# Kernel optimization log

Hardware: AMD Instinct MI355X
Metric: run time of the kernel (lower is better)

## Reference

```python
import jax, jax.numpy as jnp
import numpy as np

P = 32    # num_particles
B = 64    # batch_size
T = 100   # seq_len
W = 50    # window_length
E = 64    # act embedding dim (emb_obs=0)
H = 256   # hidden_dim
ALPHA = 0.5  # resamp_alpha


def setup_inputs() -> dict:
    key = jax.random.key(0)
    ks = jax.random.split(key, 12)
    def lin(k, fan_in, shape):
        return jax.random.normal(k, shape, jnp.float32) / np.sqrt(fan_in).astype(np.float32)
    u = jax.random.uniform(ks[4], (T, B, P, P), jnp.float32, 1e-6, 1.0 - 1e-6)
    return {
        "prev_window": jax.random.normal(ks[0], (B, T, W), jnp.float32),
        "h0": jax.random.uniform(ks[1], (P * B, H), jnp.float32),
        "c0": jax.random.uniform(ks[2], (P * B, H), jnp.float32),
        "eps": jax.random.normal(ks[3], (T, P * B, H), jnp.float32),
        "gumbel": -jnp.log(-jnp.log(u)),  # Gumbel noise for multinomial resampling
        "W_act": lin(ks[5], W, (W, E)), "b_act": jnp.zeros((E,), jnp.float32),
        "W_ih": lin(ks[6], E, (E, 5 * H)), "b_ih": jnp.zeros((5 * H,), jnp.float32),
        "W_hh": lin(ks[7], H, (H, 5 * H)), "b_hh": jnp.zeros((5 * H,), jnp.float32),
        "W_obs": lin(ks[8], H + E, (H + E, 1)), "b_obs": jnp.zeros((1,), jnp.float32),
        "W_lab": lin(ks[9], H, (H, 1)), "b_lab": jnp.zeros((1,), jnp.float32),
    }


def reference(prev_window, h0, c0, eps, gumbel, W_act, b_act, W_ih, b_ih,
              W_hh, b_hh, W_obs, b_obs, W_lab, b_lab):
    # act embedding, tiled over particles (particle-major, matching torch repeat)
    emb = jax.nn.relu(prev_window @ W_act + b_act)          # [B,T,E]
    xs = jnp.swapaxes(jnp.tile(emb, (P, 1, 1)), 0, 1)       # [T,P*B,E]
    p0 = jnp.full((P * B, 1), np.log(1.0 / P), jnp.float32)

    barange = jnp.arange(B)

    def step(carry, inputs):
        h, c, p = carry                                      # [PB,H],[PB,H],[PB,1]
        x, eps_t, g_t = inputs                               # [PB,E],[PB,H],[B,P,P]
        gates = x @ W_ih + b_ih + h @ W_hh + b_hh            # [PB,5H]
        i, f, g, o, var = jnp.split(gates, 5, axis=1)
        mu = jax.nn.sigmoid(f) * c + jax.nn.sigmoid(i) * jnp.tanh(g)
        c1 = mu + jax.nn.softplus(var) * eps_t               # stochastic cell (reparameterize)
        h1 = jax.nn.sigmoid(o) * jnp.tanh(c1)
        # observation log-likelihood per particle
        logpdf = jnp.concatenate([h1, x], axis=1) @ W_obs + b_obs  # [PB,1]
        p1 = jax.nn.log_softmax((p + logpdf).reshape(P, B), axis=0)  # [P,B]
        # soft resampling: q = alpha*w + (1-alpha)/P, sample via Gumbel-argmax
        w1 = jnp.exp(p1)
        logits = jnp.log(ALPHA * w1 + (1.0 - ALPHA) / P)     # [P_src,B]
        idx = jnp.argmax(logits.T[:, None, :] + g_t, axis=-1).T  # [P_new,B]
        h_new = h1.reshape(P, B, H)[idx, barange[None, :]]   # [P,B,H]
        c_new = c1.reshape(P, B, H)[idx, barange[None, :]]
        w = w1[idx, barange[None, :]]                        # [P,B]
        w = w / (ALPHA * w + (1.0 - ALPHA) / P)              # importance correction
        p_new = jax.nn.log_softmax(jnp.log(w), axis=0)
        h_new = h_new.reshape(P * B, H)
        c_new = c_new.reshape(P * B, H)
        p_new = p_new.reshape(P * B, 1)
        return (h_new, c_new, p_new), (h_new, p_new)

    _, (hs, ps) = jax.lax.scan(step, (h0, c0, p0), (xs, eps, gumbel))
    # hs: [T,PB,H], ps: [T,PB,1]; dropout rate 0 -> identity
    prob = ps.reshape(T, P, B, 1)
    out = hs.reshape(T, P, B, H)
    y = jnp.sum(out * jnp.exp(prob), axis=1)                 # weighted particle mean [T,B,H]
    y_out = jax.nn.sigmoid(y @ W_lab + b_lab)                # [T,B,1]
    pf_out = jax.nn.sigmoid(hs @ W_lab + b_lab)              # [T,PB,1]
    return y_out, pf_out
```

## Files before the change

### kernel.cpp

```cpp
#include <hip/hip_runtime.h>
#include <hip/hip_bf16.h>
#include <cstddef>
#include <cstdint>

#define PP 32
#define BB 64
#define TT 100
#define WW 50
#define EE 64
#define HH 256

typedef float f4 __attribute__((ext_vector_type(4)));
typedef __attribute__((ext_vector_type(8))) short short8;
typedef __attribute__((ext_vector_type(4))) float f32x4;

__device__ __forceinline__ float sigm(float x) { return 1.0f / (1.0f + expf(-x)); }
__device__ __forceinline__ float splus(float x) {
    return fmaxf(x, 0.0f) + log1pf(expf(-fabsf(x)));
}
__device__ __forceinline__ unsigned short bfh(float x) {
    __hip_bfloat16 h = __float2bfloat16(x);
    return *reinterpret_cast<unsigned short*>(&h);
}
__device__ __forceinline__ float bff(unsigned short u) {
    __hip_bfloat16 h; *reinterpret_cast<unsigned short*>(&h) = u;
    return __bfloat162float(h);
}

__global__ __launch_bounds__(256) void k_emb(
    const float* __restrict__ pw, const float* __restrict__ w_act,
    const float* __restrict__ b_act, const float* __restrict__ w_obs,
    const float* __restrict__ b_obs,
    unsigned short* __restrict__ embh, unsigned short* __restrict__ embl,
    float* __restrict__ xobs)
{
    int tid = threadIdx.x;
    int sub = tid >> 6;
    int e   = tid & 63;
    int bt  = blockIdx.x * 4 + sub;
    int b = bt / TT, t = bt % TT;

    __shared__ float pws[4][WW + 2];
    if (e < WW) pws[sub][e] = pw[(size_t)bt * WW + e];
    __syncthreads();

    float acc = b_act[e];
    #pragma unroll 5
    for (int w = 0; w < WW; ++w) acc += pws[sub][w] * w_act[w * EE + e];
    float r = fmaxf(acc, 0.0f);

    unsigned short uh = bfh(r);
    embh[((size_t)t * BB + b) * EE + e] = uh;
    embl[((size_t)t * BB + b) * EE + e] = bfh(r - bff(uh));

    float xv = r * w_obs[HH + e];
    #pragma unroll
    for (int d = 1; d < 64; d <<= 1) xv += __shfl_xor(xv, d);
    if (e == 0) xobs[t * BB + b] = xv + b_obs[0];
}

__global__ __launch_bounds__(256) void k_packB(
    const float* __restrict__ W_ih, const float* __restrict__ W_hh,
    unsigned short* __restrict__ Bp)
{
    int i = blockIdx.x * 256 + threadIdx.x;
    int colp = i / 51200;  int r = i - colp * 51200;
    int bidx = r / 2560;   r -= bidx * 2560;
    int g    = r / 512;    r -= g * 512;
    int lane = r >> 3;     int e = r & 7;

    int c = (bidx < 10) ? bidx : (bidx - 10);
    int k = c * 32 + (lane >> 4) * 8 + e;
    int col = g * HH + colp * 16 + (lane & 15);
    float w = (k < HH) ? W_hh[(size_t)k * 1280 + col]
                       : W_ih[(size_t)(k - HH) * 1280 + col];
    unsigned short uh = bfh(w);
    Bp[i] = (bidx < 10) ? uh : bfh(w - bff(uh));
}

__global__ __launch_bounds__(256) void k_split0(
    const float* __restrict__ h0, const float* __restrict__ c0,
    unsigned short* __restrict__ hh, unsigned short* __restrict__ hl,
    float* __restrict__ cc)
{
    int i = blockIdx.x * 256 + threadIdx.x;
    float v = h0[i];
    unsigned short uh = bfh(v);
    hh[i] = uh;
    hl[i] = bfh(v - bff(uh));
    cc[i] = c0[i];
}

__global__ __launch_bounds__(256, 2) void s1_mfma(
    const unsigned short* __restrict__ Bp,
    const unsigned short* __restrict__ embh_t, const unsigned short* __restrict__ embl_t,
    const unsigned short* __restrict__ hh_in, const unsigned short* __restrict__ hl_in,
    const float* __restrict__ c_in,
    unsigned short* __restrict__ hh_out, unsigned short* __restrict__ hl_out,
    float* __restrict__ c_out,
    const int* __restrict__ gidx,
    const float* __restrict__ b_ih, const float* __restrict__ b_hh,
    const float* __restrict__ w_obs, const float* __restrict__ w_lab,
    const float* __restrict__ eps_t,
    float* __restrict__ dpo, float* __restrict__ dpl)
{
    __shared__ short8 BhL[3200];

    const int tid  = threadIdx.x;
    const int rp   = blockIdx.x & 31;
    const int cp   = blockIdx.x >> 5;
    const int lane = tid & 63;
    const int w    = tid >> 6;
    const int lh   = lane & 15;
    const int kq   = lane >> 4;
    const int R0   = rp * 64 + w * 16;

    {
        const short8* src = (const short8*)Bp + (size_t)cp * 6400;
        for (int s = tid; s < 3200; s += 256) BhL[s] = src[s];
    }

    const int myrow = R0 + lh;
    const int sr    = gidx ? gidx[myrow] : myrow;
    const size_t hoff = (size_t)sr * 512 + (size_t)kq * 16;
    const size_t eoff = (size_t)(myrow & 63) * 128 + (size_t)kq * 16;

    f32x4 acc[5];
    #pragma unroll
    for (int g = 0; g < 5; ++g) acc[g] = (f32x4)(0.0f);

    const char* hhp = (const char*)hh_in  + hoff;
    const char* hlp = (const char*)hl_in  + hoff;
    const char* ehp = (const char*)embh_t + eoff;
    const char* elp = (const char*)embl_t + eoff;
    const short8* bslab = (const short8*)Bp + (size_t)cp * 6400 + lane;

    __syncthreads();

    #pragma unroll
    for (int cs = 0; cs < 10; ++cs) {
        short8 Ah, Al;
        if (cs < 8) {
            Ah = *(const short8*)(hhp + cs * 64);
            Al = *(const short8*)(hlp + cs * 64);
        } else {
            Ah = *(const short8*)(ehp + (cs - 8) * 64);
            Al = *(const short8*)(elp + (cs - 8) * 64);
        }
        short8 Bh[5], Bl[5];
        #pragma unroll
        for (int g = 0; g < 5; ++g) {
            Bh[g] = BhL[(cs * 5 + g) * 64 + lane];
            Bl[g] = bslab[((cs + 10) * 5 + g) * 64];
        }
        #pragma unroll
        for (int g = 0; g < 5; ++g)
            acc[g] = __builtin_amdgcn_mfma_f32_16x16x32_bf16(Ah, Bh[g], acc[g], 0, 0, 0);
        #pragma unroll
        for (int g = 0; g < 5; ++g)
            acc[g] = __builtin_amdgcn_mfma_f32_16x16x32_bf16(Ah, Bl[g], acc[g], 0, 0, 0);
        #pragma unroll
        for (int g = 0; g < 5; ++g)
            acc[g] = __builtin_amdgcn_mfma_f32_16x16x32_bf16(Al, Bh[g], acc[g], 0, 0, 0);
    }

    const int hcol = cp * 16 + lh;
    float bsum[5];
    #pragma unroll
    for (int g = 0; g < 5; ++g) bsum[g] = b_ih[g * HH + hcol] + b_hh[g * HH + hcol];
    const float wobs_l = w_obs[hcol];
    const float wlab_l = w_lab[hcol];

    #pragma unroll
    for (int reg = 0; reg < 4; ++reg) {
        int row = R0 + kq * 4 + reg;
        int sr2 = gidx ? gidx[row] : row;
        float cpv = c_in[(size_t)sr2 * HH + hcol];
        float ep  = eps_t[(size_t)row * HH + hcol];

        float gi = acc[0][reg] + bsum[0];
        float gf = acc[1][reg] + bsum[1];
        float gg = acc[2][reg] + bsum[2];
        float go = acc[3][reg] + bsum[3];
        float gv = acc[4][reg] + bsum[4];

        float mu  = sigm(gf) * cpv + sigm(gi) * tanhf(gg);
        float c1v = mu + splus(gv) * ep;
        float h1v = sigm(go) * tanhf(c1v);

        c_out[(size_t)row * HH + hcol] = c1v;
        unsigned short uh = bfh(h1v);
        hh_out[(size_t)row * HH + hcol] = uh;
        hl_out[(size_t)row * HH + hcol] = bfh(h1v - bff(uh));

        float po = h1v * wobs_l, pl = h1v * wlab_l;
        po += __shfl_xor(po, 1); po += __shfl_xor(po, 2);
        po += __shfl_xor(po, 4); po += __shfl_xor(po, 8);
        pl += __shfl_xor(pl, 1); pl += __shfl_xor(pl, 2);
        pl += __shfl_xor(pl, 4); pl += __shfl_xor(pl, 8);
        if (lh == 0) {
            dpo[cp * 2048 + row] = po;
            dpl[cp * 2048 + row] = pl;
        }
    }
}

__global__ __launch_bounds__(256) void s2_kernel(
    const float* __restrict__ dpo, const float* __restrict__ dpl,
    const float* __restrict__ xobs_t, const float* __restrict__ g_t,
    const float* __restrict__ b_lab,
    float* __restrict__ p_buf, int first,
    int* __restrict__ gidx_next,
    float* __restrict__ y_out_t, float* __restrict__ pf_out_t)
{
    int b   = blockIdx.x;
    int tid = threadIdx.x;

    __shared__ float gt[PP][PP + 1];
    __shared__ float lg[PP];
    __shared__ float w1s[PP];
    __shared__ float lgt[PP];
    __shared__ float pnew[PP];
    __shared__ float dpart[PP];
    __shared__ int   idxs[PP];

    {
        f4 v = ((const f4*)(g_t + (size_t)b * 1024))[tid];
        int p = tid >> 3, j0 = (tid & 7) * 4;
        gt[p][j0 + 0] = v.x; gt[p][j0 + 1] = v.y;
        gt[p][j0 + 2] = v.z; gt[p][j0 + 3] = v.w;
    }

    int p = tid >> 3, j = tid & 7;
    {
        int o = p * BB + b;
        float s = dpo[j * 2048 + o] + dpo[(j + 8) * 2048 + o];
        s += __shfl_xor(s, 1); s += __shfl_xor(s, 2); s += __shfl_xor(s, 4);
        if (j == 0) {
            float pprev = first ? -3.4657359027997265f : p_buf[o];
            lg[p] = pprev + s + xobs_t[b];
        }
    }
    __syncthreads();

    if (tid < 32) {
        float v = lg[tid];
        float m = v;
        #pragma unroll
        for (int d = 1; d < 32; d <<= 1) m = fmaxf(m, __shfl_xor(m, d));
        float e = expf(v - m), se = e;
        #pragma unroll
        for (int d = 1; d < 32; d <<= 1) se += __shfl_xor(se, d);
        float l1 = v - m - logf(se);
        float w1 = expf(l1);
        w1s[tid] = w1;
        lgt[tid] = logf(0.5f * w1 + 0.015625f);
    }
    __syncthreads();

    if (tid < 32) {
        int p2 = tid;
        float best = -INFINITY; int bi = 0;
        #pragma unroll 8
        for (int jj = 0; jj < 32; ++jj) {
            float val = lgt[jj] + gt[p2][jj];
            if (val > best) { best = val; bi = jj; }
        }
        idxs[p2] = bi;
        gidx_next[p2 * BB + b] = bi * BB + b;

        float wv = w1s[bi];
        wv = wv / (0.5f * wv + 0.015625f);
        float lw = logf(wv);
        float m2 = lw;
        #pragma unroll
        for (int d = 1; d < 32; d <<= 1) m2 = fmaxf(m2, __shfl_xor(m2, d));
        float e2 = expf(lw - m2), s2 = e2;
        #pragma unroll
        for (int d = 1; d < 32; d <<= 1) s2 += __shfl_xor(s2, d);
        float pn = lw - m2 - logf(s2);
        pnew[p2] = pn;
        p_buf[p2 * BB + b] = pn;
    }
    __syncthreads();

    {
        int src = idxs[p] * BB + b;
        float d = dpl[j * 2048 + src] + dpl[(j + 8) * 2048 + src];
        d += __shfl_xor(d, 1); d += __shfl_xor(d, 2); d += __shfl_xor(d, 4);
        if (j == 0) dpart[p] = d;
    }
    __syncthreads();

    if (tid < 32) {
        float dd = dpart[tid];
        float bl = b_lab[0];
        pf_out_t[tid * BB + b] = 1.0f / (1.0f + expf(-(dd + bl)));
        float contrib = expf(pnew[tid]) * dd;
        #pragma unroll
        for (int d = 1; d < 32; d <<= 1) contrib += __shfl_xor(contrib, d);
        if (tid == 0) y_out_t[b] = 1.0f / (1.0f + expf(-(contrib + bl)));
    }
}

extern "C" void kernel_launch(void* const* d_in, const int* in_sizes, int n_in,
                              void* d_out, int out_size, void* d_ws, size_t ws_size,
                              hipStream_t stream)
{
    const float* prev_window = (const float*)d_in[0];
    const float* h0    = (const float*)d_in[1];
    const float* c0    = (const float*)d_in[2];
    const float* eps   = (const float*)d_in[3];
    const float* gum   = (const float*)d_in[4];
    const float* W_act = (const float*)d_in[5];
    const float* b_act = (const float*)d_in[6];
    const float* W_ih  = (const float*)d_in[7];
    const float* b_ih  = (const float*)d_in[8];
    const float* W_hh  = (const float*)d_in[9];
    const float* b_hh  = (const float*)d_in[10];
    const float* W_obs = (const float*)d_in[11];
    const float* b_obs = (const float*)d_in[12];
    const float* W_lab = (const float*)d_in[13];
    const float* b_lab = (const float*)d_in[14];

    float* out = (float*)d_out;
    char* w = (char*)d_ws;

    unsigned short* Bp   = (unsigned short*)(w);
    unsigned short* embh = (unsigned short*)(w + 1638400);
    unsigned short* embl = (unsigned short*)(w + 2457600);
    unsigned short* hhA  = (unsigned short*)(w + 3276800);
    unsigned short* hlA  = (unsigned short*)(w + 4325376);
    unsigned short* hhB  = (unsigned short*)(w + 5373952);
    unsigned short* hlB  = (unsigned short*)(w + 6422528);
    float*  cA   = (float*)(w + 7471104);
    float*  cB   = (float*)(w + 9568256);
    float*  xobs = (float*)(w + 11665408);
    float*  pbuf = (float*)(w + 11691008);
    int*    gidx = (int*)(w + 11699200);
    float*  dpo  = (float*)(w + 11707392);
    float*  dpl  = (float*)(w + 11838464);

    k_emb<<<1600, 256, 0, stream>>>(prev_window, W_act, b_act, W_obs, b_obs,
                                    embh, embl, xobs);
    k_packB<<<3200, 256, 0, stream>>>(W_ih, W_hh, Bp);
    k_split0<<<2048, 256, 0, stream>>>(h0, c0, hhA, hlA, cA);

    for (int t = 0; t < TT; ++t) {
        const unsigned short* hh_in = (t & 1) ? hhB : hhA;
        const unsigned short* hl_in = (t & 1) ? hlB : hlA;
        const float*          c_in  = (t & 1) ? cB  : cA;
        unsigned short* hh_out = (t & 1) ? hhA : hhB;
        unsigned short* hl_out = (t & 1) ? hlA : hlB;
        float*          c_out  = (t & 1) ? cA  : cB;

        s1_mfma<<<512, 256, 0, stream>>>(
            Bp, embh + (size_t)t * 4096, embl + (size_t)t * 4096,
            hh_in, hl_in, c_in, hh_out, hl_out, c_out,
            (t == 0) ? nullptr : gidx,
            b_ih, b_hh, W_obs, W_lab,
            eps + (size_t)t * 524288,
            dpo, dpl);

        s2_kernel<<<64, 256, 0, stream>>>(
            dpo, dpl, xobs + t * BB, gum + (size_t)t * 65536,
            b_lab, pbuf, (t == 0) ? 1 : 0, gidx,
            out + (size_t)t * BB,
            out + (size_t)TT * BB + (size_t)t * PP * BB);
    }
}
```

Before: 2.405 ms.

## Precompute input-gate projection x@W_ih for all timesteps outside the recurrence

The embedding contribution to the gates does not depend on the recurrent state and is identical across particles, so it is now computed once per timestep and batch in fp32 by a new pre-pass kernel. The per-step MFMA kernel then runs 8 K-chunks instead of 10 and adds the precomputed term in its epilogue. This cuts the per-step matrix work and the shared-memory B slab, and the input term is now exact fp32 rather than split-bf16. The trade-offs are an extra kernel launch up front, a larger workspace (about 33 MB), and an extra global read of the precomputed values per step.

```diff
diff --git a/kernel.cpp b/kernel.cpp
--- a/kernel.cpp
+++ b/kernel.cpp
@@ -31,8 +31,7 @@
     const float* __restrict__ pw, const float* __restrict__ w_act,
     const float* __restrict__ b_act, const float* __restrict__ w_obs,
     const float* __restrict__ b_obs,
-    unsigned short* __restrict__ embh, unsigned short* __restrict__ embl,
-    float* __restrict__ xobs)
+    float* __restrict__ emb, float* __restrict__ xobs)
 {
     int tid = threadIdx.x;
     int sub = tid >> 6;
@@ -48,15 +47,58 @@
     #pragma unroll 5
     for (int w = 0; w < WW; ++w) acc += pws[sub][w] * w_act[w * EE + e];
     float r = fmaxf(acc, 0.0f);
-
-    unsigned short uh = bfh(r);
-    embh[((size_t)t * BB + b) * EE + e] = uh;
-    embl[((size_t)t * BB + b) * EE + e] = bfh(r - bff(uh));
+    emb[((size_t)t * BB + b) * EE + e] = r;
 
     float xv = r * w_obs[HH + e];
     #pragma unroll
     for (int d = 1; d < 64; d <<= 1) xv += __shfl_xor(xv, d);
     if (e == 0) xobs[t * BB + b] = xv + b_obs[0];
+}
+
+__global__ __launch_bounds__(256) void k_embW(
+    const float* __restrict__ emb, const float* __restrict__ W_ih,
+    float* __restrict__ embW)
+{
+    int t  = blockIdx.x / 16;
+    int cp = blockIdx.x - (blockIdx.x / 16) * 16;
+    int tid = threadIdx.x;
+
+    __shared__ float le[64][65];
+    __shared__ float lw[64][80];
+
+    {
+        const f4* src = (const f4*)(emb + (size_t)t * 4096);
+        for (int i = tid; i < 1024; i += 256) {
+            f4 v = src[i];
+            int b = i >> 4, e0 = (i & 15) * 4;
+            le[b][e0 + 0] = v.x; le[b][e0 + 1] = v.y;
+            le[b][e0 + 2] = v.z; le[b][e0 + 3] = v.w;
+        }
+    }
+    {
+        for (int i = tid; i < 5120; i += 256) {
+            int e = i / 80, c = i - e * 80;
+            int g = c >> 4, lh = c & 15;
+            lw[e][c] = W_ih[(size_t)e * 1280 + g * 256 + cp * 16 + lh];
+        }
+    }
+    __syncthreads();
+
+    int lh = tid & 15, bq = tid >> 4;
+    #pragma unroll
+    for (int g = 0; g < 5; ++g) {
+        float a0 = 0, a1 = 0, a2 = 0, a3 = 0;
+        #pragma unroll
+        for (int e = 0; e < 64; ++e) {
+            float wv = lw[e][g * 16 + lh];
+            a0 += le[bq * 4 + 0][e] * wv;
+            a1 += le[bq * 4 + 1][e] * wv;
+            a2 += le[bq * 4 + 2][e] * wv;
+            a3 += le[bq * 4 + 3][e] * wv;
+        }
+        f4 o = {a0, a1, a2, a3};
+        *(f4*)&embW[(((size_t)t * 16 + cp) * 5 + g) * 1024 + lh * 64 + bq * 4] = o;
+    }
 }
 
 __global__ __launch_bounds__(256) void k_packB(
@@ -93,7 +135,7 @@
 
 __global__ __launch_bounds__(256, 2) void s1_mfma(
     const unsigned short* __restrict__ Bp,
-    const unsigned short* __restrict__ embh_t, const unsigned short* __restrict__ embl_t,
+    const float* __restrict__ embW_t,
     const unsigned short* __restrict__ hh_in, const unsigned short* __restrict__ hl_in,
     const float* __restrict__ c_in,
     unsigned short* __restrict__ hh_out, unsigned short* __restrict__ hl_out,
@@ -104,7 +146,7 @@
     const float* __restrict__ eps_t,
     float* __restrict__ dpo, float* __restrict__ dpl)
 {
-    __shared__ short8 BhL[3200];
+    __shared__ short8 BhL[2560];
 
     const int tid  = threadIdx.x;
     const int rp   = blockIdx.x & 31;
@@ -117,36 +159,27 @@
 
     {
         const short8* src = (const short8*)Bp + (size_t)cp * 6400;
-        for (int s = tid; s < 3200; s += 256) BhL[s] = src[s];
+        for (int s = tid; s < 2560; s += 256) BhL[s] = src[s];
     }
 
     const int myrow = R0 + lh;
     const int sr    = gidx ? gidx[myrow] : myrow;
     const size_t hoff = (size_t)sr * 512 + (size_t)kq * 16;
-    const size_t eoff = (size_t)(myrow & 63) * 128 + (size_t)kq * 16;
 
     f32x4 acc[5];
     #pragma unroll
     for (int g = 0; g < 5; ++g) acc[g] = (f32x4)(0.0f);
 
-    const char* hhp = (const char*)hh_in  + hoff;
-    const char* hlp = (const char*)hl_in  + hoff;
-    const char* ehp = (const char*)embh_t + eoff;
-    const char* elp = (const char*)embl_t + eoff;
+    const char* hhp = (const char*)hh_in + hoff;
+    const char* hlp = (const char*)hl_in + hoff;
     const short8* bslab = (const short8*)Bp + (size_t)cp * 6400 + lane;
 
     __syncthreads();
 
     #pragma unroll
-    for (int cs = 0; cs < 10; ++cs) {
-        short8 Ah, Al;
-        if (cs < 8) {
-            Ah = *(const short8*)(hhp + cs * 64);
-            Al = *(const short8*)(hlp + cs * 64);
-        } else {
-            Ah = *(const short8*)(ehp + (cs - 8) * 64);
-            Al = *(const short8*)(elp + (cs - 8) * 64);
-        }
+    for (int cs = 0; cs < 8; ++cs) {
+        short8 Ah = *(const short8*)(hhp + cs * 64);
+        short8 Al = *(const short8*)(hlp + cs * 64);
         short8 Bh[5], Bl[5];
         #pragma unroll
         for (int g = 0; g < 5; ++g) {
@@ -170,6 +203,11 @@
     for (int g = 0; g < 5; ++g) bsum[g] = b_ih[g * HH + hcol] + b_hh[g * HH + hcol];
     const float wobs_l = w_obs[hcol];
     const float wlab_l = w_lab[hcol];
+
+    f4 ew[5];
+    #pragma unroll
+    for (int g = 0; g < 5; ++g)
+        ew[g] = *(const f4*)&embW_t[((size_t)cp * 5 + g) * 1024 + lh * 64 + w * 16 + kq * 4];
 
     #pragma unroll
     for (int reg = 0; reg < 4; ++reg) {
@@ -178,11 +216,11 @@
         float cpv = c_in[(size_t)sr2 * HH + hcol];
         float ep  = eps_t[(size_t)row * HH + hcol];
 
-        float gi = acc[0][reg] + bsum[0];
-        float gf = acc[1][reg] + bsum[1];
-        float gg = acc[2][reg] + bsum[2];
-        float go = acc[3][reg] + bsum[3];
-        float gv = acc[4][reg] + bsum[4];
+        float gi = acc[0][reg] + bsum[0] + ew[0][reg];
+        float gf = acc[1][reg] + bsum[1] + ew[1][reg];
+        float gg = acc[2][reg] + bsum[2] + ew[2][reg];
+        float go = acc[3][reg] + bsum[3] + ew[3][reg];
+        float gv = acc[4][reg] + bsum[4] + ew[4][reg];
 
         float mu  = sigm(gf) * cpv + sigm(gi) * tanhf(gg);
         float c1v = mu + splus(gv) * ep;
@@ -327,22 +365,23 @@
     char* w = (char*)d_ws;
 
     unsigned short* Bp   = (unsigned short*)(w);
-    unsigned short* embh = (unsigned short*)(w + 1638400);
-    unsigned short* embl = (unsigned short*)(w + 2457600);
-    unsigned short* hhA  = (unsigned short*)(w + 3276800);
-    unsigned short* hlA  = (unsigned short*)(w + 4325376);
-    unsigned short* hhB  = (unsigned short*)(w + 5373952);
-    unsigned short* hlB  = (unsigned short*)(w + 6422528);
-    float*  cA   = (float*)(w + 7471104);
-    float*  cB   = (float*)(w + 9568256);
-    float*  xobs = (float*)(w + 11665408);
-    float*  pbuf = (float*)(w + 11691008);
-    int*    gidx = (int*)(w + 11699200);
-    float*  dpo  = (float*)(w + 11707392);
-    float*  dpl  = (float*)(w + 11838464);
+    float*  emb  = (float*)(w + 1638400);
+    float*  embW = (float*)(w + 3276800);
+    unsigned short* hhA  = (unsigned short*)(w + 36044800);
+    unsigned short* hlA  = (unsigned short*)(w + 37093376);
+    unsigned short* hhB  = (unsigned short*)(w + 38141952);
+    unsigned short* hlB  = (unsigned short*)(w + 39190528);
+    float*  cA   = (float*)(w + 40239104);
+    float*  cB   = (float*)(w + 42336256);
+    float*  xobs = (float*)(w + 44433408);
+    float*  pbuf = (float*)(w + 44459008);
+    int*    gidx = (int*)(w + 44467200);
+    float*  dpo  = (float*)(w + 44475392);
+    float*  dpl  = (float*)(w + 44606464);
 
     k_emb<<<1600, 256, 0, stream>>>(prev_window, W_act, b_act, W_obs, b_obs,
-                                    embh, embl, xobs);
+                                    emb, xobs);
+    k_embW<<<1600, 256, 0, stream>>>(emb, W_ih, embW);
     k_packB<<<3200, 256, 0, stream>>>(W_ih, W_hh, Bp);
     k_split0<<<2048, 256, 0, stream>>>(h0, c0, hhA, hlA, cA);
 
@@ -355,7 +394,7 @@
         float*          c_out  = (t & 1) ? cA  : cB;
 
         s1_mfma<<<512, 256, 0, stream>>>(
-            Bp, embh + (size_t)t * 4096, embl + (size_t)t * 4096,
+            Bp, embW + (size_t)t * 81920,
             hh_in, hl_in, c_in, hh_out, hl_out, c_out,
             (t == 0) ? nullptr : gidx,
             b_ih, b_hh, W_obs, W_lab,
```

New measurement: 2.449 ms. Within noise of the previous version (+1.8%).

## Fuse resampling step into next LSTM step kernel, halving per-step launches

Applied to the files above, without the earlier changes.

The separate per-timestep resampling kernel is removed. Each block of the next step's MFMA kernel now redundantly recomputes the log-softmax and Gumbel-argmax for its own particle row, so it can gather h and c directly without a gidx round-trip. Output writes for step t-1 (pf, y) are spread across designated blocks, and a final s2_fin handles the last step. The partial dot products move to a row-major [row][16] layout with double-buffered dpo/dpl/pbuf. This removes about 100 kernel launches and their serialization, at the cost of redundant softmax and argmax work in all 512 blocks. It also makes the y computation in one block serial, which could lengthen the critical path.

```diff
diff --git a/kernel.cpp b/kernel.cpp
--- a/kernel.cpp
+++ b/kernel.cpp
@@ -91,20 +91,28 @@
     cc[i] = c0[i];
 }
 
-__global__ __launch_bounds__(256, 2) void s1_mfma(
+__global__ __launch_bounds__(256, 2) void g_step(
     const unsigned short* __restrict__ Bp,
     const unsigned short* __restrict__ embh_t, const unsigned short* __restrict__ embl_t,
     const unsigned short* __restrict__ hh_in, const unsigned short* __restrict__ hl_in,
     const float* __restrict__ c_in,
     unsigned short* __restrict__ hh_out, unsigned short* __restrict__ hl_out,
     float* __restrict__ c_out,
-    const int* __restrict__ gidx,
+    const float* __restrict__ dpo_prev, const float* __restrict__ dpl_prev,
+    float* __restrict__ dpo_cur, float* __restrict__ dpl_cur,
+    const float* __restrict__ pb_prev, float* __restrict__ pb_cur,
+    const float* __restrict__ xobs_prev, const float* __restrict__ gum_prev,
     const float* __restrict__ b_ih, const float* __restrict__ b_hh,
     const float* __restrict__ w_obs, const float* __restrict__ w_lab,
+    const float* __restrict__ b_lab,
     const float* __restrict__ eps_t,
-    float* __restrict__ dpo, float* __restrict__ dpl)
+    float* __restrict__ y_prev, float* __restrict__ pf_prev,
+    int skip, int rfirst)
 {
     __shared__ short8 BhL[3200];
+    __shared__ float lgS[PP][65];
+    __shared__ float lgtS[PP][65];
+    __shared__ int   idxS[BB];
 
     const int tid  = threadIdx.x;
     const int rp   = blockIdx.x & 31;
@@ -120,10 +128,107 @@
         for (int s = tid; s < 3200; s += 256) BhL[s] = src[s];
     }
 
-    const int myrow = R0 + lh;
-    const int sr    = gidx ? gidx[myrow] : myrow;
-    const size_t hoff = (size_t)sr * 512 + (size_t)kq * 16;
-    const size_t eoff = (size_t)(myrow & 63) * 128 + (size_t)kq * 16;
+    if (!skip) {
+        #pragma unroll
+        for (int k = 0; k < 8; ++k) {
+            int e = tid + k * 256;
+            int p = e >> 6, b = e & 63;
+            const f4* q = (const f4*)(dpo_prev + (size_t)e * 16);
+            f4 q0 = q[0], q1 = q[1], q2 = q[2], q3 = q[3];
+            float s = ((q0.x+q0.y)+(q0.z+q0.w)) + ((q1.x+q1.y)+(q1.z+q1.w))
+                    + ((q2.x+q2.y)+(q2.z+q2.w)) + ((q3.x+q3.y)+(q3.z+q3.w));
+            float pprev = rfirst ? -3.4657359027997265f : pb_prev[e];
+            lgS[p][b] = pprev + s + xobs_prev[b];
+        }
+        __syncthreads();
+
+        {
+            int half = lane >> 5, pl = lane & 31;
+            #pragma unroll
+            for (int it = 0; it < 8; ++it) {
+                int b = w * 16 + it * 2 + half;
+                float v = lgS[pl][b];
+                float m = v;
+                #pragma unroll
+                for (int d = 1; d < 32; d <<= 1) m = fmaxf(m, __shfl_xor(m, d));
+                float e = expf(v - m), se = e;
+                #pragma unroll
+                for (int d = 1; d < 32; d <<= 1) se += __shfl_xor(se, d);
+                float l1 = v - m - logf(se);
+                float w1 = expf(l1);
+                lgS[pl][b]  = w1;
+                lgtS[pl][b] = logf(0.5f * w1 + 0.015625f);
+            }
+        }
+        __syncthreads();
+
+        {
+            int b = tid >> 2, jq = tid & 3;
+            const float* gb = gum_prev + (size_t)b * 1024 + rp * 32;
+            float best = -INFINITY; int bi = 0;
+            #pragma unroll
+            for (int u = 0; u < 8; ++u) {
+                int jj = jq * 8 + u;
+                float val = lgtS[jj][b] + gb[jj];
+                if (val > best) { best = val; bi = jj; }
+            }
+            #pragma unroll
+            for (int d = 1; d <= 2; d <<= 1) {
+                float ov = __shfl_xor(best, d);
+                int   oj = __shfl_xor(bi, d);
+                if (ov > best || (ov == best && oj < bi)) { best = ov; bi = oj; }
+            }
+            if (jq == 0) idxS[b] = bi;
+        }
+        __syncthreads();
+
+        if (cp == 0 && tid < 64) {
+            int b = tid;
+            float wv = lgS[idxS[b]][b];
+            wv = wv / (0.5f * wv + 0.015625f);
+            pb_cur[rp * 64 + b] = logf(wv);
+        }
+        if (cp == 1) {
+            int b = tid >> 2, cq = tid & 3;
+            int srcrow = idxS[b] * 64 + b;
+            f4 vq = ((const f4*)(dpl_prev + (size_t)srcrow * 16))[cq];
+            float dsum = (vq.x + vq.y) + (vq.z + vq.w);
+            dsum += __shfl_xor(dsum, 1);
+            dsum += __shfl_xor(dsum, 2);
+            if (cq == 0) pf_prev[rp * 64 + b] = 1.0f / (1.0f + expf(-(dsum + b_lab[0])));
+        }
+        if (cp == 2 && rp == 0) {
+            int b = tid >> 2, pq = tid & 3;
+            float aw = 0.0f, ww = 0.0f;
+            for (int u = 0; u < 8; ++u) {
+                int p = pq * 8 + u;
+                const float* gb2 = gum_prev + (size_t)b * 1024 + p * 32;
+                float best = -INFINITY; int bi = 0;
+                for (int jj = 0; jj < 32; ++jj) {
+                    float val = lgtS[jj][b] + gb2[jj];
+                    if (val > best) { best = val; bi = jj; }
+                }
+                float wv = lgS[bi][b];
+                wv = wv / (0.5f * wv + 0.015625f);
+                const f4* q = (const f4*)(dpl_prev + (size_t)(bi * 64 + b) * 16);
+                f4 q0 = q[0], q1 = q[1], q2 = q[2], q3 = q[3];
+                float dsum = ((q0.x+q0.y)+(q0.z+q0.w)) + ((q1.x+q1.y)+(q1.z+q1.w))
+                           + ((q2.x+q2.y)+(q2.z+q2.w)) + ((q3.x+q3.y)+(q3.z+q3.w));
+                aw += wv * dsum; ww += wv;
+            }
+            aw += __shfl_xor(aw, 1); aw += __shfl_xor(aw, 2);
+            ww += __shfl_xor(ww, 1); ww += __shfl_xor(ww, 2);
+            if (pq == 0) y_prev[b] = 1.0f / (1.0f + expf(-(aw / ww + b_lab[0])));
+        }
+    } else {
+        if (tid < 64) idxS[tid] = rp;
+        __syncthreads();
+    }
+
+    const int b_a = w * 16 + lh;
+    const int srr = idxS[b_a] * 64 + b_a;
+    const size_t hoff = (size_t)srr * 512 + (size_t)kq * 16;
+    const size_t eoff = (size_t)b_a * 128 + (size_t)kq * 16;
 
     f32x4 acc[5];
     #pragma unroll
@@ -134,8 +239,6 @@
     const char* ehp = (const char*)embh_t + eoff;
     const char* elp = (const char*)embl_t + eoff;
     const short8* bslab = (const short8*)Bp + (size_t)cp * 6400 + lane;
-
-    __syncthreads();
 
     #pragma unroll
     for (int cs = 0; cs < 10; ++cs) {
@@ -174,7 +277,8 @@
     #pragma unroll
     for (int reg = 0; reg < 4; ++reg) {
         int row = R0 + kq * 4 + reg;
-        int sr2 = gidx ? gidx[row] : row;
+        int b2  = w * 16 + kq * 4 + reg;
+        int sr2 = idxS[b2] * 64 + b2;
         float cpv = c_in[(size_t)sr2 * HH + hcol];
         float ep  = eps_t[(size_t)row * HH + hcol];
 
@@ -199,18 +303,16 @@
         pl += __shfl_xor(pl, 1); pl += __shfl_xor(pl, 2);
         pl += __shfl_xor(pl, 4); pl += __shfl_xor(pl, 8);
         if (lh == 0) {
-            dpo[cp * 2048 + row] = po;
-            dpl[cp * 2048 + row] = pl;
-        }
-    }
-}
-
-__global__ __launch_bounds__(256) void s2_kernel(
+            dpo_cur[row * 16 + cp] = po;
+            dpl_cur[row * 16 + cp] = pl;
+        }
+    }
+}
+
+__global__ __launch_bounds__(256) void s2_fin(
     const float* __restrict__ dpo, const float* __restrict__ dpl,
     const float* __restrict__ xobs_t, const float* __restrict__ g_t,
-    const float* __restrict__ b_lab,
-    float* __restrict__ p_buf, int first,
-    int* __restrict__ gidx_next,
+    const float* __restrict__ b_lab, const float* __restrict__ p_buf,
     float* __restrict__ y_out_t, float* __restrict__ pf_out_t)
 {
     int b   = blockIdx.x;
@@ -234,12 +336,9 @@
     int p = tid >> 3, j = tid & 7;
     {
         int o = p * BB + b;
-        float s = dpo[j * 2048 + o] + dpo[(j + 8) * 2048 + o];
+        float s = dpo[o * 16 + j] + dpo[o * 16 + j + 8];
         s += __shfl_xor(s, 1); s += __shfl_xor(s, 2); s += __shfl_xor(s, 4);
-        if (j == 0) {
-            float pprev = first ? -3.4657359027997265f : p_buf[o];
-            lg[p] = pprev + s + xobs_t[b];
-        }
+        if (j == 0) lg[p] = p_buf[o] + s + xobs_t[b];
     }
     __syncthreads();
 
@@ -267,7 +366,6 @@
             if (val > best) { best = val; bi = jj; }
         }
         idxs[p2] = bi;
-        gidx_next[p2 * BB + b] = bi * BB + b;
 
         float wv = w1s[bi];
         wv = wv / (0.5f * wv + 0.015625f);
@@ -278,15 +376,13 @@
         float e2 = expf(lw - m2), s2 = e2;
         #pragma unroll
         for (int d = 1; d < 32; d <<= 1) s2 += __shfl_xor(s2, d);
-        float pn = lw - m2 - logf(s2);
-        pnew[p2] = pn;
-        p_buf[p2 * BB + b] = pn;
+        pnew[p2] = lw - m2 - logf(s2);
     }
     __syncthreads();
 
     {
         int src = idxs[p] * BB + b;
-        float d = dpl[j * 2048 + src] + dpl[(j + 8) * 2048 + src];
+        float d = dpl[src * 16 + j] + dpl[src * 16 + j + 8];
         d += __shfl_xor(d, 1); d += __shfl_xor(d, 2); d += __shfl_xor(d, 4);
         if (j == 0) dpart[p] = d;
     }
@@ -336,10 +432,12 @@
     float*  cA   = (float*)(w + 7471104);
     float*  cB   = (float*)(w + 9568256);
     float*  xobs = (float*)(w + 11665408);
-    float*  pbuf = (float*)(w + 11691008);
-    int*    gidx = (int*)(w + 11699200);
-    float*  dpo  = (float*)(w + 11707392);
-    float*  dpl  = (float*)(w + 11838464);
+    float*  pbA  = (float*)(w + 11691008);
+    float*  pbB  = (float*)(w + 11699200);
+    float*  dpoA = (float*)(w + 11707392);
+    float*  dpoB = (float*)(w + 11838464);
+    float*  dplA = (float*)(w + 11969536);
+    float*  dplB = (float*)(w + 12100608);
 
     k_emb<<<1600, 256, 0, stream>>>(prev_window, W_act, b_act, W_obs, b_obs,
                                     embh, embl, xobs);
@@ -347,25 +445,37 @@
     k_split0<<<2048, 256, 0, stream>>>(h0, c0, hhA, hlA, cA);
 
     for (int t = 0; t < TT; ++t) {
-        const unsigned short* hh_in = (t & 1) ? hhB : hhA;
-        const unsigned short* hl_in = (t & 1) ? hlB : hlA;
-        const float*          c_in  = (t & 1) ? cB  : cA;
-        unsigned short* hh_out = (t & 1) ? hhA : hhB;
-        unsigned short* hl_out = (t & 1) ? hlA : hlB;
-        float*          c_out  = (t & 1) ? cA  : cB;
-
-        s1_mfma<<<512, 256, 0, stream>>>(
+        int par = t & 1;
+        const unsigned short* hh_in = par ? hhB : hhA;
+        const unsigned short* hl_in = par ? hlB : hlA;
+        const float*          c_in  = par ? cB  : cA;
+        unsigned short* hh_out = par ? hhA : hhB;
+        unsigned short* hl_out = par ? hlA : hlB;
+        float*          c_out  = par ? cA  : cB;
+
+        float* dpoC = par ? dpoB : dpoA;
+        float* dplC = par ? dplB : dplA;
+        const float* dpoP = par ? dpoA : dpoB;
+        const float* dplP = par ? dplA : dplB;
+        float* pbC = par ? pbB : pbA;
+        const float* pbP = par ? pbA : pbB;
+
+        int tp = (t > 0) ? (t - 1) : 0;
+        g_step<<<512, 256, 0, stream>>>(
             Bp, embh + (size_t)t * 4096, embl + (size_t)t * 4096,
             hh_in, hl_in, c_in, hh_out, hl_out, c_out,
-            (t == 0) ? nullptr : gidx,
-            b_ih, b_hh, W_obs, W_lab,
+            dpoP, dplP, dpoC, dplC, pbP, pbC,
+            xobs + tp * BB, gum + (size_t)tp * 65536,
+            b_ih, b_hh, W_obs, W_lab, b_lab,
             eps + (size_t)t * 524288,
-            dpo, dpl);
-
-        s2_kernel<<<64, 256, 0, stream>>>(
-            dpo, dpl, xobs + t * BB, gum + (size_t)t * 65536,
-            b_lab, pbuf, (t == 0) ? 1 : 0, gidx,
-            out + (size_t)t * BB,
-            out + (size_t)TT * BB + (size_t)t * PP * BB);
-    }
-}
+            out + (size_t)tp * BB,
+            out + (size_t)TT * BB + (size_t)tp * PP * BB,
+            (t == 0) ? 1 : 0, (t == 1) ? 1 : 0);
+    }
+
+    s2_fin<<<64, 256, 0, stream>>>(
+        dpoB, dplB, xobs + 99 * BB, gum + (size_t)99 * 65536,
+        b_lab, pbB,
+        out + (size_t)99 * BB,
+        out + (size_t)TT * BB + (size_t)99 * PP * BB);
+}
```

After: 3.269 ms. +35.9%, slower.

## Fuse resampling step into recurrent kernel with atomic-counter grid barrier

Applied to the files above, without the earlier changes.

Merges the per-batch resampling and output kernel into the MFMA LSTM-step kernel. Each block increments a per-timestep atomic counter once its outputs are written. The first 64 blocks spin until all 512 blocks have arrived, then run the resampling logic, which halves the kernel launches per timestep. The loads of the previous cell state and the eps noise are also hoisted ahead of the MFMA loop to hide their latency. The spin-wait relies on all 512 blocks being co-resident; if they are not, the kernel can deadlock.

```diff
diff --git a/kernel.cpp b/kernel.cpp
--- a/kernel.cpp
+++ b/kernel.cpp
@@ -91,20 +91,32 @@
     cc[i] = c0[i];
 }
 
-__global__ __launch_bounds__(256, 2) void s1_mfma(
+__global__ __launch_bounds__(256, 2) void g_step(
     const unsigned short* __restrict__ Bp,
     const unsigned short* __restrict__ embh_t, const unsigned short* __restrict__ embl_t,
     const unsigned short* __restrict__ hh_in, const unsigned short* __restrict__ hl_in,
     const float* __restrict__ c_in,
     unsigned short* __restrict__ hh_out, unsigned short* __restrict__ hl_out,
     float* __restrict__ c_out,
-    const int* __restrict__ gidx,
+    const int* __restrict__ gidx_in,
+    int* __restrict__ gidx_out,
     const float* __restrict__ b_ih, const float* __restrict__ b_hh,
     const float* __restrict__ w_obs, const float* __restrict__ w_lab,
     const float* __restrict__ eps_t,
-    float* __restrict__ dpo, float* __restrict__ dpl)
+    float* __restrict__ dpo, float* __restrict__ dpl,
+    const float* __restrict__ xobs_t, const float* __restrict__ g_t,
+    const float* __restrict__ b_lab, float* __restrict__ p_buf, int first,
+    float* __restrict__ y_out_t, float* __restrict__ pf_out_t,
+    unsigned* __restrict__ cnt)
 {
     __shared__ short8 BhL[3200];
+    __shared__ float s_gt[PP][PP + 1];
+    __shared__ float s_lg[PP];
+    __shared__ float s_w1[PP];
+    __shared__ float s_lgt[PP];
+    __shared__ float s_pn[PP];
+    __shared__ float s_dp[PP];
+    __shared__ int   s_idx[PP];
 
     const int tid  = threadIdx.x;
     const int rp   = blockIdx.x & 31;
@@ -121,9 +133,21 @@
     }
 
     const int myrow = R0 + lh;
-    const int sr    = gidx ? gidx[myrow] : myrow;
+    const int sr    = gidx_in ? gidx_in[myrow] : myrow;
     const size_t hoff = (size_t)sr * 512 + (size_t)kq * 16;
     const size_t eoff = (size_t)(myrow & 63) * 128 + (size_t)kq * 16;
+
+    const int hcol = cp * 16 + lh;
+    int   srow[4];
+    float cpre[4], epre[4];
+    #pragma unroll
+    for (int reg = 0; reg < 4; ++reg) {
+        int row = R0 + kq * 4 + reg;
+        int sr2 = gidx_in ? gidx_in[row] : row;
+        srow[reg] = sr2;
+        cpre[reg] = c_in[(size_t)sr2 * HH + hcol];
+        epre[reg] = eps_t[(size_t)row * HH + hcol];
+    }
 
     f32x4 acc[5];
     #pragma unroll
@@ -164,7 +188,6 @@
             acc[g] = __builtin_amdgcn_mfma_f32_16x16x32_bf16(Al, Bh[g], acc[g], 0, 0, 0);
     }
 
-    const int hcol = cp * 16 + lh;
     float bsum[5];
     #pragma unroll
     for (int g = 0; g < 5; ++g) bsum[g] = b_ih[g * HH + hcol] + b_hh[g * HH + hcol];
@@ -174,9 +197,8 @@
     #pragma unroll
     for (int reg = 0; reg < 4; ++reg) {
         int row = R0 + kq * 4 + reg;
-        int sr2 = gidx ? gidx[row] : row;
-        float cpv = c_in[(size_t)sr2 * HH + hcol];
-        float ep  = eps_t[(size_t)row * HH + hcol];
+        float cpv = cpre[reg];
+        float ep  = epre[reg];
 
         float gi = acc[0][reg] + bsum[0];
         float gf = acc[1][reg] + bsum[1];
@@ -203,103 +225,100 @@
             dpl[cp * 2048 + row] = pl;
         }
     }
-}
-
-__global__ __launch_bounds__(256) void s2_kernel(
-    const float* __restrict__ dpo, const float* __restrict__ dpl,
-    const float* __restrict__ xobs_t, const float* __restrict__ g_t,
-    const float* __restrict__ b_lab,
-    float* __restrict__ p_buf, int first,
-    int* __restrict__ gidx_next,
-    float* __restrict__ y_out_t, float* __restrict__ pf_out_t)
-{
-    int b   = blockIdx.x;
-    int tid = threadIdx.x;
-
-    __shared__ float gt[PP][PP + 1];
-    __shared__ float lg[PP];
-    __shared__ float w1s[PP];
-    __shared__ float lgt[PP];
-    __shared__ float pnew[PP];
-    __shared__ float dpart[PP];
-    __shared__ int   idxs[PP];
-
-    {
-        f4 v = ((const f4*)(g_t + (size_t)b * 1024))[tid];
-        int p = tid >> 3, j0 = (tid & 7) * 4;
-        gt[p][j0 + 0] = v.x; gt[p][j0 + 1] = v.y;
-        gt[p][j0 + 2] = v.z; gt[p][j0 + 3] = v.w;
-    }
-
-    int p = tid >> 3, j = tid & 7;
-    {
-        int o = p * BB + b;
-        float s = dpo[j * 2048 + o] + dpo[(j + 8) * 2048 + o];
-        s += __shfl_xor(s, 1); s += __shfl_xor(s, 2); s += __shfl_xor(s, 4);
-        if (j == 0) {
-            float pprev = first ? -3.4657359027997265f : p_buf[o];
-            lg[p] = pprev + s + xobs_t[b];
-        }
-    }
+
+    __threadfence();
     __syncthreads();
-
-    if (tid < 32) {
-        float v = lg[tid];
-        float m = v;
-        #pragma unroll
-        for (int d = 1; d < 32; d <<= 1) m = fmaxf(m, __shfl_xor(m, d));
-        float e = expf(v - m), se = e;
-        #pragma unroll
-        for (int d = 1; d < 32; d <<= 1) se += __shfl_xor(se, d);
-        float l1 = v - m - logf(se);
-        float w1 = expf(l1);
-        w1s[tid] = w1;
-        lgt[tid] = logf(0.5f * w1 + 0.015625f);
-    }
-    __syncthreads();
-
-    if (tid < 32) {
-        int p2 = tid;
-        float best = -INFINITY; int bi = 0;
-        #pragma unroll 8
-        for (int jj = 0; jj < 32; ++jj) {
-            float val = lgt[jj] + gt[p2][jj];
-            if (val > best) { best = val; bi = jj; }
-        }
-        idxs[p2] = bi;
-        gidx_next[p2 * BB + b] = bi * BB + b;
-
-        float wv = w1s[bi];
-        wv = wv / (0.5f * wv + 0.015625f);
-        float lw = logf(wv);
-        float m2 = lw;
-        #pragma unroll
-        for (int d = 1; d < 32; d <<= 1) m2 = fmaxf(m2, __shfl_xor(m2, d));
-        float e2 = expf(lw - m2), s2 = e2;
-        #pragma unroll
-        for (int d = 1; d < 32; d <<= 1) s2 += __shfl_xor(s2, d);
-        float pn = lw - m2 - logf(s2);
-        pnew[p2] = pn;
-        p_buf[p2 * BB + b] = pn;
-    }
-    __syncthreads();
-
-    {
-        int src = idxs[p] * BB + b;
-        float d = dpl[j * 2048 + src] + dpl[(j + 8) * 2048 + src];
-        d += __shfl_xor(d, 1); d += __shfl_xor(d, 2); d += __shfl_xor(d, 4);
-        if (j == 0) dpart[p] = d;
-    }
-    __syncthreads();
-
-    if (tid < 32) {
-        float dd = dpart[tid];
-        float bl = b_lab[0];
-        pf_out_t[tid * BB + b] = 1.0f / (1.0f + expf(-(dd + bl)));
-        float contrib = expf(pnew[tid]) * dd;
-        #pragma unroll
-        for (int d = 1; d < 32; d <<= 1) contrib += __shfl_xor(contrib, d);
-        if (tid == 0) y_out_t[b] = 1.0f / (1.0f + expf(-(contrib + bl)));
+    if (tid == 0)
+        __hip_atomic_fetch_add(cnt, 1u, __ATOMIC_RELEASE, __HIP_MEMORY_SCOPE_AGENT);
+
+    if (blockIdx.x < BB) {
+        if (tid == 0) {
+            while (__hip_atomic_load(cnt, __ATOMIC_ACQUIRE,
+                                     __HIP_MEMORY_SCOPE_AGENT) < 512u)
+                __builtin_amdgcn_s_sleep(2);
+        }
+        __syncthreads();
+        __threadfence();
+
+        const int b = blockIdx.x;
+
+        {
+            f4 v = ((const f4*)(g_t + (size_t)b * 1024))[tid];
+            int p = tid >> 3, j0 = (tid & 7) * 4;
+            s_gt[p][j0 + 0] = v.x; s_gt[p][j0 + 1] = v.y;
+            s_gt[p][j0 + 2] = v.z; s_gt[p][j0 + 3] = v.w;
+        }
+
+        int p = tid >> 3, j = tid & 7;
+        {
+            int o = p * BB + b;
+            float s = dpo[j * 2048 + o] + dpo[(j + 8) * 2048 + o];
+            s += __shfl_xor(s, 1); s += __shfl_xor(s, 2); s += __shfl_xor(s, 4);
+            if (j == 0) {
+                float pprev = first ? -3.4657359027997265f : p_buf[o];
+                s_lg[p] = pprev + s + xobs_t[b];
+            }
+        }
+        __syncthreads();
+
+        if (tid < 32) {
+            float v = s_lg[tid];
+            float m = v;
+            #pragma unroll
+            for (int d = 1; d < 32; d <<= 1) m = fmaxf(m, __shfl_xor(m, d));
+            float e = expf(v - m), se = e;
+            #pragma unroll
+            for (int d = 1; d < 32; d <<= 1) se += __shfl_xor(se, d);
+            float l1 = v - m - logf(se);
+            float w1 = expf(l1);
+            s_w1[tid]  = w1;
+            s_lgt[tid] = logf(0.5f * w1 + 0.015625f);
+        }
+        __syncthreads();
+
+        if (tid < 32) {
+            int p2 = tid;
+            float best = -INFINITY; int bi = 0;
+            #pragma unroll 8
+            for (int jj = 0; jj < 32; ++jj) {
+                float val = s_lgt[jj] + s_gt[p2][jj];
+                if (val > best) { best = val; bi = jj; }
+            }
+            s_idx[p2] = bi;
+            gidx_out[p2 * BB + b] = bi * BB + b;
+
+            float wv = s_w1[bi];
+            wv = wv / (0.5f * wv + 0.015625f);
+            float lw = logf(wv);
+            float m2 = lw;
+            #pragma unroll
+            for (int d = 1; d < 32; d <<= 1) m2 = fmaxf(m2, __shfl_xor(m2, d));
+            float e2 = expf(lw - m2), s2 = e2;
+            #pragma unroll
+            for (int d = 1; d < 32; d <<= 1) s2 += __shfl_xor(s2, d);
+            float pn = lw - m2 - logf(s2);
+            s_pn[p2] = pn;
+            p_buf[p2 * BB + b] = pn;
+        }
+        __syncthreads();
+
+        {
+            int src = s_idx[p] * BB + b;
+            float d = dpl[j * 2048 + src] + dpl[(j + 8) * 2048 + src];
+            d += __shfl_xor(d, 1); d += __shfl_xor(d, 2); d += __shfl_xor(d, 4);
+            if (j == 0) s_dp[p] = d;
+        }
+        __syncthreads();
+
+        if (tid < 32) {
+            float dd = s_dp[tid];
+            float bl = b_lab[0];
+            pf_out_t[tid * BB + b] = 1.0f / (1.0f + expf(-(dd + bl)));
+            float contrib = expf(s_pn[tid]) * dd;
+            #pragma unroll
+            for (int d = 1; d < 32; d <<= 1) contrib += __shfl_xor(contrib, d);
+            if (tid == 0) y_out_t[b] = 1.0f / (1.0f + expf(-(contrib + bl)));
+        }
     }
 }
 
@@ -340,32 +359,34 @@
     int*    gidx = (int*)(w + 11699200);
     float*  dpo  = (float*)(w + 11707392);
     float*  dpl  = (float*)(w + 11838464);
-
+    unsigned* cnts = (unsigned*)(w + 11969536);
+
+    hipMemsetAsync(cnts, 0, 512, stream);
     k_emb<<<1600, 256, 0, stream>>>(prev_window, W_act, b_act, W_obs, b_obs,
                                     embh, embl, xobs);
     k_packB<<<3200, 256, 0, stream>>>(W_ih, W_hh, Bp);
     k_split0<<<2048, 256, 0, stream>>>(h0, c0, hhA, hlA, cA);
 
     for (int t = 0; t < TT; ++t) {
-        const unsigned short* hh_in = (t & 1) ? hhB : hhA;
-        const unsigned short* hl_in = (t & 1) ? hlB : hlA;
-        const float*          c_in  = (t & 1) ? cB  : cA;
-        unsigned short* hh_out = (t & 1) ? hhA : hhB;
-        unsigned short* hl_out = (t & 1) ? hlA : hlB;
-        float*          c_out  = (t & 1) ? cA  : cB;
-
-        s1_mfma<<<512, 256, 0, stream>>>(
+        int par = t & 1;
+        const unsigned short* hh_in = par ? hhB : hhA;
+        const unsigned short* hl_in = par ? hlB : hlA;
+        const float*          c_in  = par ? cB  : cA;
+        unsigned short* hh_out = par ? hhA : hhB;
+        unsigned short* hl_out = par ? hlA : hlB;
+        float*          c_out  = par ? cA  : cB;
+
+        g_step<<<512, 256, 0, stream>>>(
             Bp, embh + (size_t)t * 4096, embl + (size_t)t * 4096,
             hh_in, hl_in, c_in, hh_out, hl_out, c_out,
-            (t == 0) ? nullptr : gidx,
+            (t == 0) ? nullptr : gidx, gidx,
             b_ih, b_hh, W_obs, W_lab,
             eps + (size_t)t * 524288,
-            dpo, dpl);
-
-        s2_kernel<<<64, 256, 0, stream>>>(
-            dpo, dpl, xobs + t * BB, gum + (size_t)t * 65536,
-            b_lab, pbuf, (t == 0) ? 1 : 0, gidx,
+            dpo, dpl,
+            xobs + t * BB, gum + (size_t)t * 65536,
+            b_lab, pbuf, (t == 0) ? 1 : 0,
             out + (size_t)t * BB,
-            out + (size_t)TT * BB + (size_t)t * PP * BB);
-    }
-}
+            out + (size_t)TT * BB + (size_t)t * PP * BB,
+            cnts + t);
+    }
+}
```

New measurement: 8.988 ms. 3.74x slower.
